# Kernel optimization log

Measured on AMD Instinct MI355X. Metric: run time of the kernel, lower is better.

## Reference

```python
import jax, jax.numpy as jnp
import numpy as np

B, T, I, H, V, E = 512, 256, 256, 1024, 1024, 8
FUT = 64


def _lstm_cell(x_t, h, c, Wih, Whh, b):
    # PyTorch gate order: i, f, g, o. b = b_ih + b_hh (mathematically identical).
    z = x_t @ Wih.T + h @ Whh.T + b  # [B, 4H]
    i, f, g, o = jnp.split(z, 4, axis=-1)
    i = jax.nn.sigmoid(i)
    f = jax.nn.sigmoid(f)
    g = jnp.tanh(g)
    o = jax.nn.sigmoid(o)
    c_new = f * c + i * g
    h_new = o * jnp.tanh(c_new)
    return h_new, c_new


def setup_inputs() -> dict:
    key = jax.random.key(0)
    ks = jax.random.split(key, 10)
    s = 0.02
    return {
        "x_hist": jax.random.normal(ks[0], (B, T, I), jnp.float32),
        "enc_Wih": jax.random.normal(ks[1], (4 * H, I), jnp.float32) * s,
        "enc_Whh": jax.random.normal(ks[2], (4 * H, H), jnp.float32) * s,
        "enc_b": jnp.zeros((4 * H,), jnp.float32),
        "embed_W": jax.random.normal(ks[3], (V, E), jnp.float32),
        "dec_Wih": jax.random.normal(ks[4], (4 * H, E), jnp.float32) * s,
        "dec_Whh": jax.random.normal(ks[5], (4 * H, H), jnp.float32) * s,
        "dec_b": jnp.zeros((4 * H,), jnp.float32),
        "fc_W": jax.random.normal(ks[6], (V, H), jnp.float32) * s,
        "fc_b": jnp.zeros((V,), jnp.float32),
        "future_len": FUT,
    }


def reference(x_hist, enc_Wih, enc_Whh, enc_b, embed_W, dec_Wih, dec_Whh,
              dec_b, fc_W, fc_b, future_len):
    bsz = x_hist.shape[0]
    h0 = jnp.zeros((bsz, enc_Whh.shape[1]), x_hist.dtype)
    c0 = jnp.zeros_like(h0)

    # Encoder LSTM over history (batch_first): scan over time.
    def enc_step(carry, x_t):
        h, c = carry
        h, c = _lstm_cell(x_t, h, c, enc_Wih, enc_Whh, enc_b)
        return (h, c), None

    (h, c), _ = jax.lax.scan(enc_step, (h0, c0), jnp.swapaxes(x_hist, 0, 1))

    y0 = jnp.zeros((bsz,), jnp.int32)

    def dec_step(carry, _):
        h, c, y_prev = carry
        x = embed_W[y_prev]                       # [B, E] embedding lookup
        h, c = _lstm_cell(x, h, c, dec_Wih, dec_Whh, dec_b)
        logits = h @ fc_W.T + fc_b                # [B, V]
        y = jnp.argmax(logits, axis=1).astype(jnp.int32)
        return (h, c, y), logits

    _, logits = jax.lax.scan(dec_step, (h, c, y0), None, length=future_len)
    return jnp.swapaxes(logits, 0, 1)             # [B, future_len, V]
```

## Files before the change

kernel.cpp:

```cpp
#include <hip/hip_runtime.h>
#include <cmath>

typedef __attribute__((ext_vector_type(8))) short short8;
typedef __attribute__((ext_vector_type(4))) float f32x4;

#define B_SZ 512
#define T_SZ 256
#define I_SZ 256
#define H_SZ 1024
#define V_SZ 1024
#define E_SZ 8
#define FUT 64

#define KVE 3840
#define KVD 3328
#define KVF 3072
#define APE 2560
#define APD 2176

static __device__ __forceinline__ ushort f2bf(float v) {
    uint32_t u = __float_as_uint(v);
    uint32_t r = (u + 0x7fffu + ((u >> 16) & 1u)) >> 16;
    return (ushort)r;
}
static __device__ __forceinline__ float bf2f(ushort b) {
    return __uint_as_float(((uint32_t)b) << 16);
}

#define GLD16(gp, lp)                                                          \
    __builtin_amdgcn_global_load_lds(                                         \
        (const __attribute__((address_space(1))) void*)(gp),                  \
        (__attribute__((address_space(3))) void*)(lp), 16, 0, 0)

template<int MFR, int NFR, int NTPX, int NK, int T1, int T2,
         int O0, int O1, int O2, bool GATES>
__global__ __launch_bounds__(256) void gemm_step(
    const ushort* __restrict__ A, int astr,
    const ushort* __restrict__ W, int kv,
    const float* __restrict__ bias,
    float* __restrict__ c,
    ushort* __restrict__ hdest, int ldh,
    const float* __restrict__ xsrc, ushort* __restrict__ xdest,
    float* __restrict__ out, int ldo)
{
    constexpr int ABUF = MFR * 2048;
    constexpr int WBUF = NFR * 2048;
    __shared__ __align__(16) ushort lds[4 * (ABUF + WBUF)];

    const int tid = threadIdx.x;
    const int lane = tid & 63;
    const int wid = tid >> 6;
    const int wm = wid >> 1, wn = wid & 1;
    const int l15 = lane & 15, lq = lane >> 4;
    const int l7 = lane & 7, l3 = lane >> 3;

    const int flat = blockIdx.x;
    const int xcd = flat & 7, slot = flat >> 3;
    const int n_tile = xcd * NTPX + (slot % NTPX);
    const int m_tile = slot / NTPX;
    const int m0 = m_tile * (MFR * 32);
    const int n0 = n_tile * (NFR * 32);

    f32x4 acc[MFR][NFR];
#pragma unroll
    for (int m = 0; m < MFR; ++m)
#pragma unroll
        for (int n = 0; n < NFR; ++n) { f32x4 z = {0.f, 0.f, 0.f, 0.f}; acc[m][n] = z; }

    auto STAGE = [&](int p, int bufi) {
        const int off = p < T1 ? O0 : (p < T2 ? O1 : O2);
        const int kc = p * 64;
        ushort* ab = &lds[bufi * ABUF];
        ushort* wb = &lds[4 * ABUF + bufi * WBUF];
#pragma unroll
        for (int i = 0; i < MFR; ++i) {
            const int rowg = (i * 4 + wid) * 8;
            const int row = rowg + l3;
            GLD16(A + (size_t)(m0 + row) * astr + kc + off + ((l7 ^ l3) * 8),
                  ab + rowg * 64);
        }
#pragma unroll
        for (int i = 0; i < NFR; ++i) {
            const int rowg = (i * 4 + wid) * 8;
            const int row = rowg + l3;
            GLD16(W + (size_t)(n0 + row) * kv + kc + ((l7 ^ l3) * 8),
                  wb + rowg * 64);
        }
    };
    auto COMPUTE = [&](int bufi) {
        const ushort* ab = &lds[bufi * ABUF];
        const ushort* wb = &lds[4 * ABUF + bufi * WBUF];
#pragma unroll
        for (int kk = 0; kk < 2; ++kk) {
            short8 af[MFR], wf[NFR];
#pragma unroll
            for (int m = 0; m < MFR; ++m) {
                const int row = wm * (MFR * 16) + m * 16 + l15;
                af[m] = *(const short8*)
                    &ab[row * 64 + (((kk * 4 + lq) ^ (row & 7)) * 8)];
            }
#pragma unroll
            for (int n = 0; n < NFR; ++n) {
                const int row = wn * (NFR * 16) + n * 16 + l15;
                wf[n] = *(const short8*)
                    &wb[row * 64 + (((kk * 4 + lq) ^ (row & 7)) * 8)];
            }
            __builtin_amdgcn_s_setprio(1);
#pragma unroll
            for (int m = 0; m < MFR; ++m)
#pragma unroll
                for (int n = 0; n < NFR; ++n)
                    acc[m][n] = __builtin_amdgcn_mfma_f32_16x16x32_bf16(
                        af[m], wf[n], acc[m][n], 0, 0, 0);
            __builtin_amdgcn_s_setprio(0);
        }
    };

    STAGE(0, 0);
    if (NK > 1) STAGE(1, 1);
    if (NK > 2) STAGE(2, 2);
#pragma unroll 1
    for (int p0 = 0; p0 < NK; p0 += 4) {
#pragma unroll
        for (int j = 0; j < 4; ++j) {
            const int p = p0 + j;
            if (p < NK) {
                if (p + 2 < NK) {
                    if constexpr (MFR + NFR == 4)
                        asm volatile("s_waitcnt vmcnt(8)" ::: "memory");
                    else
                        asm volatile("s_waitcnt vmcnt(4)" ::: "memory");
                } else if (p + 1 < NK) {
                    if constexpr (MFR + NFR == 4)
                        asm volatile("s_waitcnt vmcnt(4)" ::: "memory");
                    else
                        asm volatile("s_waitcnt vmcnt(2)" ::: "memory");
                } else {
                    asm volatile("s_waitcnt vmcnt(0)" ::: "memory");
                }
                __builtin_amdgcn_s_barrier();
                if (p + 3 < NK) STAGE(p + 3, (j + 3) & 3);
                COMPUTE(j);
            }
        }
    }

    if constexpr (GATES) {
        float* zs = (float*)&lds[0];
        __syncthreads();
#pragma unroll
        for (int m = 0; m < MFR; ++m)
#pragma unroll
            for (int n = 0; n < NFR; ++n)
#pragma unroll
                for (int r = 0; r < 4; ++r)
                    zs[(wm * 32 + m * 16 + lq * 4 + r) * 65 +
                       wn * 32 + n * 16 + l15] = acc[m][n][r];
        __syncthreads();

        const int row = tid & 63;
        const int jl0 = (tid >> 6) * 4;
        const int grow = m0 + row;
        const int jg = n_tile * 16 + jl0;
        const f32x4 bi4 = *(const f32x4*)&bias[n0 + jl0];
        const f32x4 bf4 = *(const f32x4*)&bias[n0 + 16 + jl0];
        const f32x4 bg4 = *(const f32x4*)&bias[n0 + 32 + jl0];
        const f32x4 bo4 = *(const f32x4*)&bias[n0 + 48 + jl0];
        f32x4 cv = *(f32x4*)&c[(size_t)grow * H_SZ + jg];
        ushort hh[4], hl[4];
#pragma unroll
        for (int jj = 0; jj < 4; ++jj) {
            const float zi = zs[row * 65 + jl0 + jj] + bi4[jj];
            const float zf = zs[row * 65 + 16 + jl0 + jj] + bf4[jj];
            const float zg = zs[row * 65 + 32 + jl0 + jj] + bg4[jj];
            const float zo = zs[row * 65 + 48 + jl0 + jj] + bo4[jj];
            const float ig = 1.f / (1.f + expf(-zi));
            const float fg = 1.f / (1.f + expf(-zf));
            const float gg = tanhf(zg);
            const float og = 1.f / (1.f + expf(-zo));
            const float cn = fg * cv[jj] + ig * gg;
            cv[jj] = cn;
            const float hv = og * tanhf(cn);
            hh[jj] = f2bf(hv);
            hl[jj] = f2bf(hv - bf2f(hh[jj]));
        }
        *(f32x4*)&c[(size_t)grow * H_SZ + jg] = cv;
        ushort* hd = hdest + (size_t)grow * ldh + jg;
        uint hv2[2], lv2[2];
        hv2[0] = (uint)hh[0] | ((uint)hh[1] << 16);
        hv2[1] = (uint)hh[2] | ((uint)hh[3] << 16);
        lv2[0] = (uint)hl[0] | ((uint)hl[1] << 16);
        lv2[1] = (uint)hl[2] | ((uint)hl[3] << 16);
        *(uint*)&hd[0] = hv2[0];
        *(uint*)&hd[2] = hv2[1];
        *(uint*)&hd[1024] = lv2[0];
        *(uint*)&hd[1026] = lv2[1];

        if (xdest) {
            const int idx = flat * 256 + tid;
            const int b = idx >> 8, i = idx & 255;
            const float v = xsrc[(size_t)b * (T_SZ * I_SZ) + i];
            const ushort hi = f2bf(v), lo = f2bf(v - bf2f(hi));
            xdest[(size_t)b * APE + i] = hi;
            xdest[(size_t)b * APE + 256 + i] = lo;
        }
    } else {
#pragma unroll
        for (int m = 0; m < MFR; ++m)
#pragma unroll
            for (int n = 0; n < NFR; ++n) {
                const int col = n0 + wn * (NFR * 16) + n * 16 + l15;
                const float bv = bias[col];
#pragma unroll
                for (int r = 0; r < 4; ++r) {
                    const int row = m0 + wm * (MFR * 16) + m * 16 + lq * 4 + r;
                    out[(size_t)row * ldo + col] = acc[m][n][r] + bv;
                }
            }
    }
}

__global__ __launch_bounds__(256) void argmax_embed(
    const float* __restrict__ logits, int ldl,
    const float* __restrict__ embed_W,
    ushort* __restrict__ xdest)
{
    const int b = blockIdx.x;
    const float* row = logits + (size_t)b * ldl;
    const int tid = threadIdx.x;
    float best = -INFINITY;
    int bi = V_SZ;
#pragma unroll
    for (int v = tid; v < V_SZ; v += 256) {
        const float x = row[v];
        if (x > best) { best = x; bi = v; }
    }
    __shared__ float sv[256];
    __shared__ int si[256];
    sv[tid] = best; si[tid] = bi;
    __syncthreads();
    for (int s = 128; s > 0; s >>= 1) {
        if (tid < s) {
            const float ov = sv[tid + s]; const int oi = si[tid + s];
            if (ov > sv[tid] || (ov == sv[tid] && oi < si[tid])) { sv[tid] = ov; si[tid] = oi; }
        }
        __syncthreads();
    }
    if (tid < E_SZ) {
        const int yb = si[0];
        const float v = embed_W[(size_t)yb * E_SZ + tid];
        const ushort hi = f2bf(v), lo = f2bf(v - bf2f(hi));
        ushort* xd = xdest + (size_t)b * APD;
        xd[tid] = hi;
        xd[8 + tid] = hi;
        xd[16 + tid] = lo;
    }
}

__global__ void pack_enc(const float* __restrict__ Wih, const float* __restrict__ Whh,
                         const float* __restrict__ b, ushort* __restrict__ Wp,
                         float* __restrict__ bp)
{
    const int k = blockIdx.x * 256 + threadIdx.x;
    const int np = blockIdx.y;
    const int orig = ((np >> 4) & 3) * H_SZ + (np >> 6) * 16 + (np & 15);
    float v; bool lo = false;
    if (k < 256)        v = Wih[(size_t)orig * I_SZ + k];
    else if (k < 512) { v = Wih[(size_t)orig * I_SZ + k - 256]; lo = true; }
    else if (k < 768)   v = Wih[(size_t)orig * I_SZ + k - 512];
    else if (k < 1792)  v = Whh[(size_t)orig * H_SZ + k - 768];
    else if (k < 2816) { v = Whh[(size_t)orig * H_SZ + k - 1792]; lo = true; }
    else                v = Whh[(size_t)orig * H_SZ + k - 2816];
    const ushort hi = f2bf(v);
    Wp[(size_t)np * KVE + k] = lo ? f2bf(v - bf2f(hi)) : hi;
    if (k == 0) bp[np] = b[orig];
}

__global__ void pack_dec(const float* __restrict__ Wih, const float* __restrict__ Whh,
                         const float* __restrict__ b, ushort* __restrict__ Wp,
                         float* __restrict__ bp)
{
    const int k = blockIdx.x * 256 + threadIdx.x;
    const int np = blockIdx.y;
    const int orig = ((np >> 4) & 3) * H_SZ + (np >> 6) * 16 + (np & 15);
    float v = 0.f; bool lo = false; bool zero = false;
    if (k < 8)            v = Wih[(size_t)orig * E_SZ + k];
    else if (k < 16)    { v = Wih[(size_t)orig * E_SZ + k - 8]; lo = true; }
    else if (k < 24)      v = Wih[(size_t)orig * E_SZ + k - 16];
    else if (k < 128)     zero = true;
    else if (k < 1152)    v = Whh[(size_t)orig * H_SZ + k - 128];
    else if (k < 2176)  { v = Whh[(size_t)orig * H_SZ + k - 1152]; lo = true; }
    else if (k < 3200)    v = Whh[(size_t)orig * H_SZ + k - 2176];
    else                  zero = true;
    ushort w = 0;
    if (!zero) { const ushort hi = f2bf(v); w = lo ? f2bf(v - bf2f(hi)) : hi; }
    Wp[(size_t)np * KVD + k] = w;
    if (k == 0) bp[np] = b[orig];
}

__global__ void pack_fc(const float* __restrict__ W, ushort* __restrict__ Wp)
{
    const int k = blockIdx.x * 256 + threadIdx.x;
    const int np = blockIdx.y;
    float v; bool lo = false;
    if (k < 1024)       v = W[(size_t)np * H_SZ + k];
    else if (k < 2048) { v = W[(size_t)np * H_SZ + k - 1024]; lo = true; }
    else                v = W[(size_t)np * H_SZ + k - 2048];
    const ushort hi = f2bf(v);
    Wp[(size_t)np * KVF + k] = lo ? f2bf(v - bf2f(hi)) : hi;
}

__global__ void init_all(const float* __restrict__ x0,
                         const float* __restrict__ embed_W,
                         float* __restrict__ c,
                         ushort* __restrict__ Aenc0,
                         ushort* __restrict__ Adec0,
                         ushort* __restrict__ Adec1)
{
    const int idx = blockIdx.x * 256 + threadIdx.x;
    {
        const int b = idx >> 11, k = idx & 2047;
        Aenc0[(size_t)b * APE + 512 + k] = 0;
    }
    if (idx < B_SZ * H_SZ) c[idx] = 0.f;
    if (idx < B_SZ * I_SZ) {
        const int b = idx >> 8, i = idx & 255;
        const float v = x0[(size_t)b * (T_SZ * I_SZ) + i];
        const ushort hi = f2bf(v), lo = f2bf(v - bf2f(hi));
        Aenc0[(size_t)b * APE + i] = hi;
        Aenc0[(size_t)b * APE + 256 + i] = lo;
    }
    if (idx < B_SZ * 104) {
        const int b = idx / 104, col = 24 + idx % 104;
        Adec0[(size_t)b * APD + col] = 0;
        Adec1[(size_t)b * APD + col] = 0;
    }
    if (idx < B_SZ * 24) {
        const int b = idx / 24, col = idx % 24;
        float v;
        if (col < 8)       v = embed_W[col];
        else if (col < 16) v = embed_W[col - 8];
        else               v = embed_W[col - 16];
        const ushort hi = f2bf(v);
        Adec0[(size_t)b * APD + col] = (col < 16) ? hi : f2bf(v - bf2f(hi));
    }
}

extern "C" void kernel_launch(void* const* d_in, const int* in_sizes, int n_in,
                              void* d_out, int out_size, void* d_ws, size_t ws_size,
                              hipStream_t stream)
{
    const float* x_hist  = (const float*)d_in[0];
    const float* enc_Wih = (const float*)d_in[1];
    const float* enc_Whh = (const float*)d_in[2];
    const float* enc_b   = (const float*)d_in[3];
    const float* embed_W = (const float*)d_in[4];
    const float* dec_Wih = (const float*)d_in[5];
    const float* dec_Whh = (const float*)d_in[6];
    const float* dec_b   = (const float*)d_in[7];
    const float* fc_W    = (const float*)d_in[8];
    const float* fc_b    = (const float*)d_in[9];
    float* out = (float*)d_out;

    char* p = (char*)d_ws;
    auto alloc = [&](size_t bytes) {
        char* r = p;
        p += (bytes + 255) & ~(size_t)255;
        return r;
    };
    ushort* W_enc  = (ushort*)alloc((size_t)4096 * KVE * 2);
    ushort* W_dec  = (ushort*)alloc((size_t)4096 * KVD * 2);
    ushort* W_fc   = (ushort*)alloc((size_t)1024 * KVF * 2);
    ushort* A_enc0 = (ushort*)alloc((size_t)B_SZ * APE * 2);
    ushort* A_enc1 = (ushort*)alloc((size_t)B_SZ * APE * 2);
    ushort* A_dec0 = (ushort*)alloc((size_t)B_SZ * APD * 2);
    ushort* A_dec1 = (ushort*)alloc((size_t)B_SZ * APD * 2);
    float*  cbuf   = (float*)alloc((size_t)B_SZ * H_SZ * 4);
    float*  bpe    = (float*)alloc(4096 * 4);
    float*  bpd    = (float*)alloc(4096 * 4);

    const dim3 blk(256);
    hipLaunchKernelGGL(pack_enc, dim3(15, 4096), blk, 0, stream, enc_Wih, enc_Whh, enc_b, W_enc, bpe);
    hipLaunchKernelGGL(pack_dec, dim3(13, 4096), blk, 0, stream, dec_Wih, dec_Whh, dec_b, W_dec, bpd);
    hipLaunchKernelGGL(pack_fc,  dim3(12, 1024), blk, 0, stream, fc_W, W_fc);
    hipLaunchKernelGGL(init_all, dim3(4096), blk, 0, stream, x_hist, embed_W, cbuf, A_enc0, A_dec0, A_dec1);

    ushort* Ae[2] = {A_enc0, A_enc1};
    ushort* Ad[2] = {A_dec0, A_dec1};

    for (int t = 0; t < T_SZ; ++t) {
        ushort* hdst; int ldh; const float* xs; ushort* xd;
        if (t < T_SZ - 1) {
            hdst = Ae[(t + 1) & 1] + 512; ldh = APE;
            xs = x_hist + (size_t)(t + 1) * I_SZ;
            xd = Ae[(t + 1) & 1];
        } else {
            hdst = Ad[0] + 128; ldh = APD;
            xs = nullptr; xd = nullptr;
        }
        hipLaunchKernelGGL((gemm_step<2, 2, 8, 60, 4, 28, 0, -256, -1280, true>),
                           dim3(512), blk, 0, stream,
                           Ae[t & 1], APE, W_enc, KVE, bpe, cbuf,
                           hdst, ldh, xs, xd, (float*)nullptr, 0);
    }

    for (int t = 0; t < FUT; ++t) {
        hipLaunchKernelGGL((gemm_step<2, 2, 8, 50, 18, 50, 0, -1024, -1024, true>),
                           dim3(512), blk, 0, stream,
                           Ad[t & 1], APD, W_dec, KVD, bpd, cbuf,
                           Ad[(t + 1) & 1] + 128, APD,
                           (const float*)nullptr, (ushort*)nullptr,
                           (float*)nullptr, 0);
        float* logits = out + (size_t)t * V_SZ;
        hipLaunchKernelGGL((gemm_step<1, 1, 4, 48, 16, 48, 128, -896, -896, false>),
                           dim3(512), blk, 0, stream,
                           Ad[(t + 1) & 1], APD, W_fc, KVF, fc_b,
                           (float*)nullptr, (ushort*)nullptr, 0,
                           (const float*)nullptr, (ushort*)nullptr,
                           logits, FUT * V_SZ);
        hipLaunchKernelGGL(argmax_embed, dim3(512), blk, 0, stream,
                           logits, FUT * V_SZ, embed_W, Ad[(t + 1) & 1]);
    }
}
```

Baseline: 10.21 ms.

## Fuse argmax into FC GEMM epilogue via packed atomicMax keys

The FC GEMM epilogue now computes a per-row argmax over its 32-column tile in LDS and merges it globally with a 64-bit atomicMax on a monotonic float key packed with an inverted index, so lower indices win ties. The separate 512-block argmax kernel, which re-read the logits, becomes a tiny 16-block gather that reads the winning index, writes the split-bf16 embedding and resets the key. The aim is to cut a full logits re-read and most of a kernel's work per decode step, at the cost of an extra LDS pass, syncs and atomics in the epilogue. It also drops the s_setprio wrappers around the MFMA loop in all GEMM variants, and the non-gates epilogue is now hardcoded to a single 1x1 fragment.

```diff
diff --git a/kernel.cpp b/kernel.cpp
--- a/kernel.cpp
+++ b/kernel.cpp
@@ -25,6 +25,10 @@
 }
 static __device__ __forceinline__ float bf2f(ushort b) {
     return __uint_as_float(((uint32_t)b) << 16);
+}
+static __device__ __forceinline__ uint32_t fmono(float f) {
+    uint32_t u = __float_as_uint(f);
+    return (u & 0x80000000u) ? ~u : (u | 0x80000000u);
 }
 
 #define GLD16(gp, lp)                                                          \
@@ -41,7 +45,8 @@
     float* __restrict__ c,
     ushort* __restrict__ hdest, int ldh,
     const float* __restrict__ xsrc, ushort* __restrict__ xdest,
-    float* __restrict__ out, int ldo)
+    float* __restrict__ out, int ldo,
+    unsigned long long* __restrict__ keys)
 {
     constexpr int ABUF = MFR * 2048;
     constexpr int WBUF = NFR * 2048;
@@ -105,14 +110,12 @@
                 wf[n] = *(const short8*)
                     &wb[row * 64 + (((kk * 4 + lq) ^ (row & 7)) * 8)];
             }
-            __builtin_amdgcn_s_setprio(1);
 #pragma unroll
             for (int m = 0; m < MFR; ++m)
 #pragma unroll
                 for (int n = 0; n < NFR; ++n)
                     acc[m][n] = __builtin_amdgcn_mfma_f32_16x16x32_bf16(
                         af[m], wf[n], acc[m][n], 0, 0, 0);
-            __builtin_amdgcn_s_setprio(0);
         }
     };
 
@@ -205,56 +208,56 @@
             xdest[(size_t)b * APE + 256 + i] = lo;
         }
     } else {
-#pragma unroll
-        for (int m = 0; m < MFR; ++m)
-#pragma unroll
-            for (int n = 0; n < NFR; ++n) {
-                const int col = n0 + wn * (NFR * 16) + n * 16 + l15;
-                const float bv = bias[col];
-#pragma unroll
-                for (int r = 0; r < 4; ++r) {
-                    const int row = m0 + wm * (MFR * 16) + m * 16 + lq * 4 + r;
-                    out[(size_t)row * ldo + col] = acc[m][n][r] + bv;
+        float vals[4];
+        const int col = n0 + wn * 16 + l15;
+        const float bv = bias[col];
+#pragma unroll
+        for (int r = 0; r < 4; ++r) {
+            const int row = m0 + wm * 16 + lq * 4 + r;
+            vals[r] = acc[0][0][r] + bv;
+            out[(size_t)row * ldo + col] = vals[r];
+        }
+        if (keys) {
+            float* zs = (float*)&lds[0];
+            __syncthreads();
+#pragma unroll
+            for (int r = 0; r < 4; ++r)
+                zs[(wm * 16 + lq * 4 + r) * 33 + wn * 16 + l15] = vals[r];
+            __syncthreads();
+            if (tid < 32) {
+                const int row = tid;
+                float best = zs[row * 33];
+                int bc = 0;
+#pragma unroll
+                for (int cc = 1; cc < 32; ++cc) {
+                    const float x = zs[row * 33 + cc];
+                    if (x > best) { best = x; bc = cc; }
                 }
+                const unsigned long long key =
+                    ((unsigned long long)fmono(best) << 32) |
+                    (unsigned long long)(V_SZ - 1 - (n0 + bc));
+                atomicMax(&keys[m0 + row], key);
             }
-    }
-}
-
-__global__ __launch_bounds__(256) void argmax_embed(
-    const float* __restrict__ logits, int ldl,
+        }
+    }
+}
+
+__global__ __launch_bounds__(256) void gather_embed(
+    unsigned long long* __restrict__ keys,
     const float* __restrict__ embed_W,
     ushort* __restrict__ xdest)
 {
-    const int b = blockIdx.x;
-    const float* row = logits + (size_t)b * ldl;
-    const int tid = threadIdx.x;
-    float best = -INFINITY;
-    int bi = V_SZ;
-#pragma unroll
-    for (int v = tid; v < V_SZ; v += 256) {
-        const float x = row[v];
-        if (x > best) { best = x; bi = v; }
-    }
-    __shared__ float sv[256];
-    __shared__ int si[256];
-    sv[tid] = best; si[tid] = bi;
-    __syncthreads();
-    for (int s = 128; s > 0; s >>= 1) {
-        if (tid < s) {
-            const float ov = sv[tid + s]; const int oi = si[tid + s];
-            if (ov > sv[tid] || (ov == sv[tid] && oi < si[tid])) { sv[tid] = ov; si[tid] = oi; }
-        }
-        __syncthreads();
-    }
-    if (tid < E_SZ) {
-        const int yb = si[0];
-        const float v = embed_W[(size_t)yb * E_SZ + tid];
-        const ushort hi = f2bf(v), lo = f2bf(v - bf2f(hi));
-        ushort* xd = xdest + (size_t)b * APD;
-        xd[tid] = hi;
-        xd[8 + tid] = hi;
-        xd[16 + tid] = lo;
-    }
+    const int idx = blockIdx.x * 256 + threadIdx.x;
+    const int b = idx >> 3, e = idx & 7;
+    const unsigned long long key = keys[b];
+    const int yb = V_SZ - 1 - (int)(key & 0xffffffffu);
+    const float v = embed_W[(size_t)yb * E_SZ + e];
+    const ushort hi = f2bf(v), lo = f2bf(v - bf2f(hi));
+    ushort* xd = xdest + (size_t)b * APD;
+    xd[e] = hi;
+    xd[8 + e] = hi;
+    xd[16 + e] = lo;
+    if (e == 0) keys[b] = 0ull;
 }
 
 __global__ void pack_enc(const float* __restrict__ Wih, const float* __restrict__ Whh,
@@ -315,7 +318,8 @@
                          float* __restrict__ c,
                          ushort* __restrict__ Aenc0,
                          ushort* __restrict__ Adec0,
-                         ushort* __restrict__ Adec1)
+                         ushort* __restrict__ Adec1,
+                         unsigned long long* __restrict__ keys)
 {
     const int idx = blockIdx.x * 256 + threadIdx.x;
     {
@@ -323,6 +327,7 @@
         Aenc0[(size_t)b * APE + 512 + k] = 0;
     }
     if (idx < B_SZ * H_SZ) c[idx] = 0.f;
+    if (idx < B_SZ) keys[idx] = 0ull;
     if (idx < B_SZ * I_SZ) {
         const int b = idx >> 8, i = idx & 255;
         const float v = x0[(size_t)b * (T_SZ * I_SZ) + i];
@@ -378,12 +383,13 @@
     float*  cbuf   = (float*)alloc((size_t)B_SZ * H_SZ * 4);
     float*  bpe    = (float*)alloc(4096 * 4);
     float*  bpd    = (float*)alloc(4096 * 4);
+    unsigned long long* keys = (unsigned long long*)alloc(B_SZ * 8);
 
     const dim3 blk(256);
     hipLaunchKernelGGL(pack_enc, dim3(15, 4096), blk, 0, stream, enc_Wih, enc_Whh, enc_b, W_enc, bpe);
     hipLaunchKernelGGL(pack_dec, dim3(13, 4096), blk, 0, stream, dec_Wih, dec_Whh, dec_b, W_dec, bpd);
     hipLaunchKernelGGL(pack_fc,  dim3(12, 1024), blk, 0, stream, fc_W, W_fc);
-    hipLaunchKernelGGL(init_all, dim3(4096), blk, 0, stream, x_hist, embed_W, cbuf, A_enc0, A_dec0, A_dec1);
+    hipLaunchKernelGGL(init_all, dim3(4096), blk, 0, stream, x_hist, embed_W, cbuf, A_enc0, A_dec0, A_dec1, keys);
 
     ushort* Ae[2] = {A_enc0, A_enc1};
     ushort* Ad[2] = {A_dec0, A_dec1};
@@ -401,7 +407,8 @@
         hipLaunchKernelGGL((gemm_step<2, 2, 8, 60, 4, 28, 0, -256, -1280, true>),
                            dim3(512), blk, 0, stream,
                            Ae[t & 1], APE, W_enc, KVE, bpe, cbuf,
-                           hdst, ldh, xs, xd, (float*)nullptr, 0);
+                           hdst, ldh, xs, xd, (float*)nullptr, 0,
+                           (unsigned long long*)nullptr);
     }
 
     for (int t = 0; t < FUT; ++t) {
@@ -410,15 +417,16 @@
                            Ad[t & 1], APD, W_dec, KVD, bpd, cbuf,
                            Ad[(t + 1) & 1] + 128, APD,
                            (const float*)nullptr, (ushort*)nullptr,
-                           (float*)nullptr, 0);
+                           (float*)nullptr, 0,
+                           (unsigned long long*)nullptr);
         float* logits = out + (size_t)t * V_SZ;
         hipLaunchKernelGGL((gemm_step<1, 1, 4, 48, 16, 48, 128, -896, -896, false>),
                            dim3(512), blk, 0, stream,
                            Ad[(t + 1) & 1], APD, W_fc, KVF, fc_b,
                            (float*)nullptr, (ushort*)nullptr, 0,
                            (const float*)nullptr, (ushort*)nullptr,
-                           logits, FUT * V_SZ);
-        hipLaunchKernelGGL(argmax_embed, dim3(512), blk, 0, stream,
-                           logits, FUT * V_SZ, embed_W, Ad[(t + 1) & 1]);
-    }
-}
+                           logits, FUT * V_SZ, keys);
+        hipLaunchKernelGGL(gather_embed, dim3(16), blk, 0, stream,
+                           keys, embed_W, Ad[(t + 1) & 1]);
+    }
+}
```

Result: no change. 10.02 ms (-1.9%).
